# Kernel optimization log

Measured on AMD Instinct MI355X. Metric: run time of the kernel, lower is better.

The kernel has to match this reference:

```python
import jax, jax.numpy as jnp
import numpy as np

# Episode / graph constants
B, N, K, Q = 16, 5, 5, 5              # episodes, ways, shots, queries-per-class
NPG = 200                              # nodes per graph
DEG = 16                               # avg degree
F_DIM, H_DIM, OUT_DIM = 128, 128, 64
NS_G = B * N * K                       # 400 support graphs
NQ_G = B * N * Q                       # 400 query graphs
NS_NODES = NS_G * NPG                  # 80000
NQ_NODES = NQ_G * NPG                  # 80000
NEG_SLOPE = 0.2


def _rand_edges(key, n_nodes):
    # random in-graph source per (dst, k) slot; dst covers every node DEG times
    n_edges = n_nodes * DEG
    off = (jnp.arange(n_edges) // (NPG * DEG)) * NPG
    src = jax.random.randint(key, (n_edges,), 0, NPG) + off
    dst = jnp.repeat(jnp.arange(n_nodes), DEG)
    return jnp.stack([src, dst]).astype(jnp.int64)


def setup_inputs() -> dict:
    key = jax.random.key(0)
    ks = jax.random.split(key, 16)
    g = lambda k, shape, scale: jax.random.normal(k, shape, jnp.float32) * scale
    inp = {
        "supports_x": g(ks[0], (NS_NODES, F_DIM), 1.0),
        "queries_x": g(ks[1], (NQ_NODES, F_DIM), 1.0),
        "supports_edge_index": _rand_edges(ks[2], NS_NODES),
        "queries_edge_index": _rand_edges(ks[3], NQ_NODES),
        "supports_batch": (jnp.arange(NS_NODES) // NPG).astype(jnp.int64),
        "queries_batch": (jnp.arange(NQ_NODES) // NPG).astype(jnp.int64),
        # per-episode labels: N classes, K graphs each, local class ids 0..N-1
        "supports_y": jnp.tile(jnp.repeat(jnp.arange(N), K), B).astype(jnp.int64),
        "W1": g(ks[4], (F_DIM, H_DIM), 1.0 / np.sqrt(F_DIM)),
        "a1_src": g(ks[5], (H_DIM,), 1.0 / np.sqrt(H_DIM)),
        "a1_dst": g(ks[6], (H_DIM,), 1.0 / np.sqrt(H_DIM)),
        "b1": jnp.zeros((H_DIM,), jnp.float32),
        "W2": g(ks[7], (H_DIM, H_DIM), 1.0 / np.sqrt(H_DIM)),
        "a2_src": g(ks[8], (H_DIM,), 1.0 / np.sqrt(H_DIM)),
        "a2_dst": g(ks[9], (H_DIM,), 1.0 / np.sqrt(H_DIM)),
        "b2": jnp.zeros((H_DIM,), jnp.float32),
        "Wm1": g(ks[10], (H_DIM, H_DIM), 1.0 / np.sqrt(H_DIM)),
        "bm1": jnp.zeros((H_DIM,), jnp.float32),
        "Wm2": g(ks[11], (H_DIM, OUT_DIM), 1.0 / np.sqrt(H_DIM)),
        "bm2": jnp.zeros((OUT_DIM,), jnp.float32),
    }
    return inp


def gat_conv(x, src, dst, W, a_src, a_dst, b, n_nodes):
    """PyG GATConv, heads=1, add_self_loops=True."""
    xw = x @ W                                        # [n, H]
    loop = jnp.arange(n_nodes)
    src2 = jnp.concatenate([src, loop])
    dst2 = jnp.concatenate([dst, loop])
    e = (xw @ a_src)[src2] + (xw @ a_dst)[dst2]       # [E+n]
    e = jnp.where(e > 0, e, NEG_SLOPE * e)            # leaky_relu
    m = jax.ops.segment_max(e, dst2, num_segments=n_nodes)
    ex = jnp.exp(e - m[dst2])
    den = jax.ops.segment_sum(ex, dst2, num_segments=n_nodes)
    alpha = ex / den[dst2]                            # softmax per destination
    out = jax.ops.segment_sum(alpha[:, None] * xw[src2], dst2, num_segments=n_nodes)
    return out + b


def embed(x, edge_index, batch, n_graphs, W1, a1s, a1d, b1, W2, a2s, a2d, b2,
          Wm1, bm1, Wm2, bm2):
    n = x.shape[0]
    src, dst = edge_index[0], edge_index[1]
    h = jax.nn.relu(gat_conv(x, src, dst, W1, a1s, a1d, b1, n))
    h = jax.nn.relu(gat_conv(h, src, dst, W2, a2s, a2d, b2, n))
    h = jax.nn.relu(h @ Wm1 + bm1) @ Wm2 + bm2        # MLP
    # global mean pool
    s = jax.ops.segment_sum(h, batch, num_segments=n_graphs)
    cnt = jax.ops.segment_sum(jnp.ones((n,), h.dtype), batch, num_segments=n_graphs)
    return s / cnt[:, None]                           # [n_graphs, OUT_DIM]


def reference(supports_x, supports_edge_index, supports_batch, supports_y,
              queries_x, queries_edge_index, queries_batch,
              W1, a1_src, a1_dst, b1, W2, a2_src, a2_dst, b2,
              Wm1, bm1, Wm2, bm2):
    params = (W1, a1_src, a1_dst, b1, W2, a2_src, a2_dst, b2, Wm1, bm1, Wm2, bm2)
    emb_s = embed(supports_x, supports_edge_index, supports_batch, NS_G, *params)
    emb_q = embed(queries_x, queries_edge_index, queries_batch, NQ_G, *params)

    # class prototypes per episode: mean of supports with each (sorted) class label
    emb_s = emb_s.reshape(B, N * K, OUT_DIM)
    y = supports_y.reshape(B, N * K)
    onehot = jax.nn.one_hot(y, N, dtype=emb_s.dtype)          # [B, NK, N]
    proto = jnp.einsum("bkn,bke->bne", onehot, emb_s)
    proto = proto / onehot.sum(axis=1)[:, :, None]            # [B, N, E]

    # align queries with prototypes
    nq = N * Q                                                # queries per episode
    emb_q = emb_q.reshape(B, nq, OUT_DIM)
    rep_q = jnp.repeat(emb_q, N, axis=1)                      # repeat_interleave
    rep_p = jnp.tile(proto, (1, nq, 1))                       # repeat
    return rep_q.reshape(B * nq * N, OUT_DIM), rep_p.reshape(B * nq * N, OUT_DIM)
```

## Files before the change

### kernel.cpp

```cpp
#include <hip/hip_runtime.h>


typedef unsigned short u16;
typedef unsigned int   u32;
typedef unsigned char  u8;
typedef __attribute__((ext_vector_type(8))) short short8;
typedef __attribute__((ext_vector_type(4))) float f32x4;

#define NNODES   80000
#define DEG      16
#define NEDGES   (NNODES * DEG)
#define NGRAPH   400
#define NPG      200
#define FDIM     128
#define ODIM     64
#define NEPS     16
#define NWAY     5
#define NSHOT    5
#define NROWS    (2 * NNODES)
#define NGR2     (2 * NGRAPH)

__device__ __forceinline__ float b2f(u16 u) {
    return __uint_as_float(((u32)u) << 16);
}
__device__ __forceinline__ u16 f2b(float f) {
    u32 i = __float_as_uint(f);
    u32 r = i + 0x7FFFu + ((i >> 16) & 1u);
    return (u16)(r >> 16);
}

__global__ void detect_kernel(const u32* __restrict__ sx,
                              const int* __restrict__ ei,
                              int* __restrict__ flags)
{
    if (blockIdx.x == 0 && threadIdx.x == 0) {
        int ok32 = (ei[NEDGES + 16000] == 1000) && (ei[NEDGES + 32000] == 2000);
        flags[0] = ok32 ? 0 : 1;
        int cnt = 0;
        for (int i = 0; i < 64; i++) {
            u32 lo = sx[i] & 0xFFFFu;
            u32 e  = (lo >> 7) & 0xFFu;
            if (e >= 110u && e <= 135u) cnt++;
        }
        flags[1] = (cnt >= 32) ? 1 : 0;
    }
}

__global__ __launch_bounds__(256)
void canon_kernel(const void* __restrict__ W1, const void* __restrict__ W2,
                  const void* __restrict__ Wm1, const void* __restrict__ Wm2,
                  const void* a1s, const void* a1d, const void* b1,
                  const void* a2s, const void* a2d, const void* b2,
                  const void* bm1, const void* bm2,
                  const int* __restrict__ flags, u16* __restrict__ Wc,
                  float* __restrict__ Vc, float* __restrict__ emb)
{
    const int b = blockIdx.x, t = threadIdx.x;
    const int isb = flags[1];
    if (b < 224) {
        int idx = b * 256 + t;
        const void* src;
        int n, k, nout;
        if (idx < 16384)      { src = W1;  int l = idx;         n = l >> 7; k = l & 127; nout = 128; }
        else if (idx < 32768) { src = W2;  int l = idx - 16384; n = l >> 7; k = l & 127; nout = 128; }
        else if (idx < 49152) { src = Wm1; int l = idx - 32768; n = l >> 7; k = l & 127; nout = 128; }
        else                  { src = Wm2; int l = idx - 49152; n = l >> 7; k = l & 127; nout = 64; }
        int off = k * nout + n;
        Wc[idx] = isb ? ((const u16*)src)[off] : f2b(((const float*)src)[off]);
    } else if (b == 224) {
        for (int idx = t; idx < 960; idx += 256) {
            int g = idx >> 7, off = idx & 127;
            const void* src = (g == 0) ? a1s : (g == 1) ? a1d : (g == 2) ? b1 :
                              (g == 3) ? a2s : (g == 4) ? a2d : (g == 5) ? b2 :
                              (g == 6) ? bm1 : bm2;
            Vc[idx] = isb ? b2f(((const u16*)src)[off]) : ((const float*)src)[off];
        }
    } else {
        int i = (b - 225) * 256 + t;
        emb[i] = 0.f;
    }
}

__global__ __launch_bounds__(512)
void gemm_pack_kernel(const void* __restrict__ in0, const void* __restrict__ in1,
                      int in_mode, const int* __restrict__ flags,
                      const u16* __restrict__ Wt, const float* __restrict__ bias,
                      const float* __restrict__ avs, const float* __restrict__ avd,
                      u32* __restrict__ outP, float* __restrict__ es_g,
                      float* __restrict__ ed_g, int do_relu)
{
    __shared__ uint4 bsh[2048];

    const int t    = threadIdx.x;
    const int wv   = t >> 6;
    const int lane = t & 63;
    const int qd   = lane >> 4, md = lane & 15;

    int mode = in_mode;
    if (mode == 2) mode = flags[1];

    const size_t rowG = (size_t)blockIdx.x * 128 + wv * 16 + md;
    const int side = rowG >= NNODES;
    const size_t lrow = rowG - (side ? NNODES : 0);
    const void* in_ = side ? in1 : in0;

    short8 afr[4];
    if (mode) {
        const short* arow = (const short*)in_ + lrow * FDIM;
#pragma unroll
        for (int ks = 0; ks < 4; ks++)
            afr[ks] = *(const short8*)(arow + ks * 32 + qd * 8);
    } else {
        const float* arow = (const float*)in_ + lrow * FDIM;
#pragma unroll
        for (int ks = 0; ks < 4; ks++) {
            float4 u = *(const float4*)(arow + ks * 32 + qd * 8);
            float4 v = *(const float4*)(arow + ks * 32 + qd * 8 + 4);
            short8 tt;
            tt[0] = (short)f2b(u.x); tt[1] = (short)f2b(u.y);
            tt[2] = (short)f2b(u.z); tt[3] = (short)f2b(u.w);
            tt[4] = (short)f2b(v.x); tt[5] = (short)f2b(v.y);
            tt[6] = (short)f2b(v.z); tt[7] = (short)f2b(v.w);
            afr[ks] = tt;
        }
    }

    {
        const uint4* w4 = (const uint4*)Wt;
#pragma unroll
        for (int it = 0; it < 4; ++it) {
            int u   = it * 512 + t;
            int ctb = u >> 8, mdb = (u >> 4) & 15, ksb = (u >> 2) & 3, qdb = u & 3;
            bsh[ctb * 256 + ksb * 64 + qdb * 16 + mdb] = w4[u];
        }
    }
    __syncthreads();

    const size_t r0 = (size_t)blockIdx.x * 128 + wv * 16 + qd * 4;
    const bool has_av = (avs != nullptr);

    float sv[4] = {0.f, 0.f, 0.f, 0.f};
    float dv[4] = {0.f, 0.f, 0.f, 0.f};

    for (int ct = 0; ct < 8; ct++) {
        f32x4 acc = {0.f, 0.f, 0.f, 0.f};
#pragma unroll
        for (int ks = 0; ks < 4; ks++) {
            short8 bfr = *(const short8*)&bsh[(ct * 4 + ks) * 64 + lane];
            acc = __builtin_amdgcn_mfma_f32_16x16x32_bf16(afr[ks], bfr, acc, 0, 0, 0);
        }
        const int col = ct * 16 + md;
        const float bv  = bias ? bias[col] : 0.f;
        const float asv = has_av ? avs[col] : 0.f;
        const float adv = has_av ? avd[col] : 0.f;
#pragma unroll
        for (int i = 0; i < 4; i++) {
            float v = acc[i] + bv;
            if (do_relu) v = fmaxf(v, 0.f);
            sv[i] = fmaf(v, asv, sv[i]);
            dv[i] = fmaf(v, adv, dv[i]);
            float pr = __shfl_xor(v, 1, 64);
            if (!(md & 1)) {
                u32 pk = (u32)f2b(v) | ((u32)f2b(pr) << 16);
                outP[(r0 + i) * 64 + ct * 8 + (md >> 1)] = pk;
            }
        }
    }

    if (has_av) {
#pragma unroll
        for (int off = 1; off <= 8; off <<= 1) {
#pragma unroll
            for (int i = 0; i < 4; i++) {
                sv[i] += __shfl_xor(sv[i], off, 64);
                dv[i] += __shfl_xor(dv[i], off, 64);
            }
        }
        if (md == 0) {
#pragma unroll
            for (int i = 0; i < 4; i++) {
                es_g[r0 + i] = sv[i];
                ed_g[r0 + i] = dv[i];
            }
        }
    }
}

__global__ __launch_bounds__(512)
void gemm_pool_kernel(const u32* __restrict__ inP, const u16* __restrict__ Wt,
                      float* __restrict__ emb)
{
    __shared__ uint4 bsh[1024];
    __shared__ float psum[2][8][64];

    const int t = threadIdx.x;
    const int wv   = t >> 6;
    const int lane = t & 63;
    const int qd   = lane >> 4, md = lane & 15;

    const size_t rowA = (size_t)blockIdx.x * 128 + wv * 16 + md;
    const short* arow = (const short*)inP + rowA * FDIM;
    short8 afr[4];
#pragma unroll
    for (int ks = 0; ks < 4; ks++)
        afr[ks] = *(const short8*)(arow + ks * 32 + qd * 8);

    {
        const uint4* w4 = (const uint4*)Wt;
#pragma unroll
        for (int it = 0; it < 2; ++it) {
            int u   = it * 512 + t;
            int ctb = u >> 8, mdb = (u >> 4) & 15, ksb = (u >> 2) & 3, qdb = u & 3;
            bsh[ctb * 256 + ksb * 64 + qdb * 16 + mdb] = w4[u];
        }
    }
    __syncthreads();

    const int r0       = blockIdx.x * 128 + wv * 16 + qd * 4;
    const int g0       = (blockIdx.x * 128) / NPG;
    const int boundary = (g0 + 1) * NPG;

    for (int ct = 0; ct < 4; ct++) {
        f32x4 acc = {0.f, 0.f, 0.f, 0.f};
#pragma unroll
        for (int ks = 0; ks < 4; ks++) {
            short8 bfr = *(const short8*)&bsh[(ct * 4 + ks) * 64 + lane];
            acc = __builtin_amdgcn_mfma_f32_16x16x32_bf16(afr[ks], bfr, acc, 0, 0, 0);
        }
        float s0 = 0.f, s1 = 0.f;
#pragma unroll
        for (int i = 0; i < 4; i++) {
            if (r0 + i >= boundary) s1 += acc[i];
            else                    s0 += acc[i];
        }
        s0 += __shfl_xor(s0, 16, 64);  s1 += __shfl_xor(s1, 16, 64);
        s0 += __shfl_xor(s0, 32, 64);  s1 += __shfl_xor(s1, 32, 64);
        if (qd == 0) {
            psum[0][wv][ct * 16 + md] = s0;
            psum[1][wv][ct * 16 + md] = s1;
        }
    }
    __syncthreads();

    if (t < 128) {
        int p = t >> 6, c = t & 63;
        float s = 0.f;
#pragma unroll
        for (int w = 0; w < 8; w++) s += psum[p][w][c];
        if (p == 0 || boundary < blockIdx.x * 128 + 128)
            atomicAdd(&emb[(size_t)(g0 + p) * ODIM + c], s * (1.f / (float)NPG));
    }
}

__global__ __launch_bounds__(1024)
void gat_kernel(const u32* __restrict__ xwP, const float* __restrict__ es_g,
                const float* __restrict__ ed_g, const int* __restrict__ src0,
                const int* __restrict__ src1, const int* __restrict__ flags,
                const float* __restrict__ bias, u32* __restrict__ outH)
{
    __shared__ __align__(16) u32 xls[NPG * 64];
    __shared__ u16 alA[NPG * 18];
    __shared__ u8  slA[NPG * 20];

    const int g = blockIdx.x, t = threadIdx.x;
    const int side  = g >= NGRAPH;
    const int gbase = g * NPG;
    const int lbase = (g - (side ? NGRAPH : 0)) * NPG;
    const int* __restrict__ src = side ? src1 : src0;

    {
        const u32* gsrc = xwP + (size_t)gbase * 64;
        const int w = t >> 6, l = t & 63;
#pragma unroll
        for (int it = 0; it < 4; ++it) {
            int chunk = w + it * 16;
            if (chunk < 50) {
                __builtin_amdgcn_global_load_lds(
                    (const u32*)(gsrc + chunk * 256 + l * 4),
                    &xls[chunk * 256], 16, 0, 0);
            }
        }
    }

    if (t < 4 * NPG) {
        const int n = t >> 2, slot = t & 3;
        const int j0 = slot * 5;
        const int jn = (slot == 3) ? 2 : 5;
        const int is64 = flags[0];
        const float edn = ed_g[gbase + n];
        int   sl[5];
        float e[5];
        float mx = -1e30f;
#pragma unroll
        for (int jj = 0; jj < 5; jj++) {
            if (jj < jn) {
                int j = j0 + jj;
                int s;
                if (j == 16) {
                    s = n;
                } else {
                    int eidx = (lbase + n) * DEG + j;
                    s = (is64 ? src[2 * eidx] : src[eidx]) - lbase;
                }
                sl[jj] = s;
                float ev = es_g[gbase + s] + edn;
                ev = (ev > 0.f) ? ev : 0.2f * ev;
                e[jj] = ev;
                mx = fmaxf(mx, ev);
            }
        }
        mx = fmaxf(mx, __shfl_xor(mx, 1, 64));
        mx = fmaxf(mx, __shfl_xor(mx, 2, 64));
        float den = 0.f;
#pragma unroll
        for (int jj = 0; jj < 5; jj++) {
            if (jj < jn) {
                e[jj] = __expf(e[jj] - mx);
                den += e[jj];
            }
        }
        den += __shfl_xor(den, 1, 64);
        den += __shfl_xor(den, 2, 64);
        const float inv = 65535.f / den;
#pragma unroll
        for (int jj = 0; jj < 5; jj++) {
            if (jj < jn) {
                alA[n * 18 + j0 + jj] = (u16)(e[jj] * inv + 0.5f);
                slA[n * 20 + j0 + jj] = (u8)sl[jj];
            }
        }
    }

    __syncthreads();

    const int w = t >> 6, l = t & 63;
    const int sub = l >> 4, li = l & 15;
    const float4 bz0 = *(const float4*)&bias[8 * li];
    const float4 bz1 = *(const float4*)&bias[8 * li + 4];

    for (int p = w; p < NPG / 4; p += 16) {
        const int n = 4 * p + sub;
        float h0 = 0.f, h1 = 0.f, h2 = 0.f, h3 = 0.f;
        float h4 = 0.f, h5 = 0.f, h6 = 0.f, h7 = 0.f;
#pragma unroll 4
        for (int j = 0; j < 17; j++) {
            float a = (float)alA[n * 18 + j] * (1.f / 65535.f);
            int   s = (int)slA[n * 20 + j];
            uint4 q = *(const uint4*)&xls[s * 64 + 4 * li];
            h0 = fmaf(a, __uint_as_float(q.x << 16), h0);
            h1 = fmaf(a, __uint_as_float(q.x & 0xFFFF0000u), h1);
            h2 = fmaf(a, __uint_as_float(q.y << 16), h2);
            h3 = fmaf(a, __uint_as_float(q.y & 0xFFFF0000u), h3);
            h4 = fmaf(a, __uint_as_float(q.z << 16), h4);
            h5 = fmaf(a, __uint_as_float(q.z & 0xFFFF0000u), h5);
            h6 = fmaf(a, __uint_as_float(q.w << 16), h6);
            h7 = fmaf(a, __uint_as_float(q.w & 0xFFFF0000u), h7);
        }
        h0 = fmaxf(h0 + bz0.x, 0.f);
        h1 = fmaxf(h1 + bz0.y, 0.f);
        h2 = fmaxf(h2 + bz0.z, 0.f);
        h3 = fmaxf(h3 + bz0.w, 0.f);
        h4 = fmaxf(h4 + bz1.x, 0.f);
        h5 = fmaxf(h5 + bz1.y, 0.f);
        h6 = fmaxf(h6 + bz1.z, 0.f);
        h7 = fmaxf(h7 + bz1.w, 0.f);
        uint4 o;
        o.x = (u32)f2b(h0) | ((u32)f2b(h1) << 16);
        o.y = (u32)f2b(h2) | ((u32)f2b(h3) << 16);
        o.z = (u32)f2b(h4) | ((u32)f2b(h5) << 16);
        o.w = (u32)f2b(h6) | ((u32)f2b(h7) << 16);
        *(uint4*)&outH[(size_t)(gbase + n) * 64 + 4 * li] = o;
    }
}

__global__ __launch_bounds__(256)
void expand_kernel(const float* __restrict__ emb, const float* __restrict__ bm2,
                   const int* __restrict__ flags, void* __restrict__ out)
{
    int idx = blockIdx.x * 256 + threadIdx.x;
    const int TOT = NEPS * 125 * ODIM;
    if (idx >= TOT) return;
    int c = idx & 63;
    int tq = (idx >> 6) % 125;
    int b = idx / (125 * ODIM);
    int q = tq / NWAY, n = tq % NWAY;
    const float bb = bm2[c];
    float v0 = emb[(size_t)(NGRAPH + b * 25 + q) * ODIM + c] + bb;
    float v1 = 0.f;
#pragma unroll
    for (int k = 0; k < NSHOT; k++)
        v1 += emb[(size_t)(b * 25 + n * NSHOT + k) * ODIM + c];
    v1 = v1 * (1.f / (float)NSHOT) + bb;
    if (flags[1]) {
        ((u16*)out)[idx]       = f2b(v0);
        ((u16*)out)[TOT + idx] = f2b(v1);
    } else {
        ((float*)out)[idx]       = v0;
        ((float*)out)[TOT + idx] = v1;
    }
}

extern "C" void kernel_launch(void* const* d_in, const int* in_sizes, int n_in,
                              void* d_out, int out_size, void* d_ws, size_t ws_size,
                              hipStream_t stream)
{
    const void* sup_x  = d_in[0];
    const void* qry_x  = d_in[1];
    const int*  sup_ei = (const int*)d_in[2];
    const int*  qry_ei = (const int*)d_in[3];
    const void* W1  = d_in[7];
    const void* a1s = d_in[8];
    const void* a1d = d_in[9];
    const void* b1  = d_in[10];
    const void* W2  = d_in[11];
    const void* a2s = d_in[12];
    const void* a2d = d_in[13];
    const void* b2  = d_in[14];
    const void* Wm1 = d_in[15];
    const void* bm1 = d_in[16];
    const void* Wm2 = d_in[17];
    const void* bm2 = d_in[18];

    u32*   bufXW = (u32*)d_ws;
    u32*   bufH  = bufXW + (size_t)NROWS * 64;
    float* es_g  = (float*)(bufH + (size_t)NROWS * 64);
    float* ed_g  = es_g + NROWS;
    float* emb   = ed_g + NROWS;
    float* Vc    = emb + (size_t)NGR2 * ODIM;
    u16*   Wc    = (u16*)(Vc + 960);
    int*   flags = (int*)(Wc + 57344);

    const float* c_a1s = Vc + 0,   *c_a1d = Vc + 128, *c_b1  = Vc + 256;
    const float* c_a2s = Vc + 384, *c_a2d = Vc + 512, *c_b2  = Vc + 640;
    const float* c_bm1 = Vc + 768, *c_bm2 = Vc + 896;
    const u16* c_W1t  = Wc;
    const u16* c_W2t  = Wc + 16384;
    const u16* c_Wm1t = Wc + 32768;
    const u16* c_Wm2t = Wc + 49152;

    const int GEMM_BLOCKS = NROWS / 128;

    detect_kernel<<<1, 64, 0, stream>>>((const u32*)sup_x, sup_ei, flags);
    canon_kernel<<<425, 256, 0, stream>>>(W1, W2, Wm1, Wm2,
                                          a1s, a1d, b1, a2s, a2d, b2, bm1, bm2,
                                          flags, Wc, Vc, emb);

    const void* bufH0 = (const void*)bufH;
    const void* bufH1 = (const void*)(bufH + (size_t)NNODES * 64);

    gemm_pack_kernel<<<GEMM_BLOCKS, 512, 0, stream>>>(
        sup_x, qry_x, 2, flags, c_W1t, nullptr, c_a1s, c_a1d,
        bufXW, es_g, ed_g, 0);
    gat_kernel<<<NGR2, 1024, 0, stream>>>(
        bufXW, es_g, ed_g, sup_ei, qry_ei, flags, c_b1, bufH);

    gemm_pack_kernel<<<GEMM_BLOCKS, 512, 0, stream>>>(
        bufH0, bufH1, 1, flags, c_W2t, nullptr, c_a2s, c_a2d,
        bufXW, es_g, ed_g, 0);
    gat_kernel<<<NGR2, 1024, 0, stream>>>(
        bufXW, es_g, ed_g, sup_ei, qry_ei, flags, c_b2, bufH);

    gemm_pack_kernel<<<GEMM_BLOCKS, 512, 0, stream>>>(
        bufH0, bufH1, 1, flags, c_Wm1t, c_bm1, nullptr, nullptr,
        bufXW, es_g, ed_g, 1);

    gemm_pool_kernel<<<GEMM_BLOCKS, 512, 0, stream>>>(bufXW, c_Wm2t, emb);

    expand_kernel<<<(NEPS * 125 * ODIM + 255) / 256, 256, 0, stream>>>(
        emb, c_bm2, flags, d_out);
}
```

Measured before the change: 313.4 us.

## Swap MFMA operands, permute hidden feature order, pad LDS, use hardware bf16 pack

The GEMM epilogue now swaps the A/B operands of the MFMA so each lane holds four consecutive output columns for a single row. This allows vectorized bias and attention-vector loads, fewer cross-lane shuffles for the attention dot products, and 8-byte stores instead of shuffled 4-byte stores. To keep downstream consumers consistent, the hidden feature dimension is stored in a permuted order (semk), and the K index of W2/Wm1/Wm2 and the b1/b2 vectors are remapped to match. The weight tile in shared memory is padded by one slot every eight to reduce bank conflicts. Software bf16 rounding is replaced with the v_cvt_pk_bf16_f32 instruction, which adds correctness risk if the permutation or the rounding behavior does not match.

```diff
diff --git a/kernel.cpp b/kernel.cpp
--- a/kernel.cpp
+++ b/kernel.cpp
@@ -28,6 +28,14 @@
     u32 r = i + 0x7FFFu + ((i >> 16) & 1u);
     return (u16)(r >> 16);
 }
+__device__ __forceinline__ u32 cvtpk(float lo, float hi) {
+    u32 r;
+    asm("v_cvt_pk_bf16_f32 %0, %1, %2" : "=v"(r) : "v"(lo), "v"(hi));
+    return r;
+}
+__device__ __forceinline__ int semk(int p) {
+    return 16 * ((p >> 2) & 7) + 4 * (p >> 5) + 2 * ((p >> 1) & 1) + (p & 1);
+}
 
 __global__ void detect_kernel(const u32* __restrict__ sx,
                               const int* __restrict__ ei,
@@ -61,10 +69,10 @@
         int idx = b * 256 + t;
         const void* src;
         int n, k, nout;
-        if (idx < 16384)      { src = W1;  int l = idx;         n = l >> 7; k = l & 127; nout = 128; }
-        else if (idx < 32768) { src = W2;  int l = idx - 16384; n = l >> 7; k = l & 127; nout = 128; }
-        else if (idx < 49152) { src = Wm1; int l = idx - 32768; n = l >> 7; k = l & 127; nout = 128; }
-        else                  { src = Wm2; int l = idx - 49152; n = l >> 7; k = l & 127; nout = 64; }
+        if (idx < 16384)      { src = W1;  int l = idx;         n = l >> 7; k = l & 127;       nout = 128; }
+        else if (idx < 32768) { src = W2;  int l = idx - 16384; n = l >> 7; k = semk(l & 127); nout = 128; }
+        else if (idx < 49152) { src = Wm1; int l = idx - 32768; n = l >> 7; k = semk(l & 127); nout = 128; }
+        else                  { src = Wm2; int l = idx - 49152; n = l >> 7; k = semk(l & 127); nout = 64; }
         int off = k * nout + n;
         Wc[idx] = isb ? ((const u16*)src)[off] : f2b(((const float*)src)[off]);
     } else if (b == 224) {
@@ -73,7 +81,8 @@
             const void* src = (g == 0) ? a1s : (g == 1) ? a1d : (g == 2) ? b1 :
                               (g == 3) ? a2s : (g == 4) ? a2d : (g == 5) ? b2 :
                               (g == 6) ? bm1 : bm2;
-            Vc[idx] = isb ? b2f(((const u16*)src)[off]) : ((const float*)src)[off];
+            int soff = (g == 2 || g == 5) ? semk(off) : off;
+            Vc[idx] = isb ? b2f(((const u16*)src)[soff]) : ((const float*)src)[soff];
         }
     } else {
         int i = (b - 225) * 256 + t;
@@ -89,12 +98,13 @@
                       u32* __restrict__ outP, float* __restrict__ es_g,
                       float* __restrict__ ed_g, int do_relu)
 {
-    __shared__ uint4 bsh[2048];
+    __shared__ __align__(16) uint4 bsh[2304];
 
     const int t    = threadIdx.x;
     const int wv   = t >> 6;
     const int lane = t & 63;
     const int qd   = lane >> 4, md = lane & 15;
+    const int lofs = lane + (lane >> 3);
 
     int mode = in_mode;
     if (mode == 2) mode = flags[1];
@@ -129,59 +139,55 @@
         const uint4* w4 = (const uint4*)Wt;
 #pragma unroll
         for (int it = 0; it < 4; ++it) {
-            int u   = it * 512 + t;
-            int ctb = u >> 8, mdb = (u >> 4) & 15, ksb = (u >> 2) & 3, qdb = u & 3;
-            bsh[ctb * 256 + ksb * 64 + qdb * 16 + mdb] = w4[u];
+            int u    = it * 512 + t;
+            int ctb  = u >> 8, mdb = (u >> 4) & 15, ksb = (u >> 2) & 3, qdb = u & 3;
+            int slot = ctb * 256 + ksb * 64 + qdb * 16 + mdb;
+            bsh[slot + (slot >> 3)] = w4[u];
         }
     }
     __syncthreads();
 
-    const size_t r0 = (size_t)blockIdx.x * 128 + wv * 16 + qd * 4;
     const bool has_av = (avs != nullptr);
-
-    float sv[4] = {0.f, 0.f, 0.f, 0.f};
-    float dv[4] = {0.f, 0.f, 0.f, 0.f};
+    float sv = 0.f, dv = 0.f;
 
     for (int ct = 0; ct < 8; ct++) {
         f32x4 acc = {0.f, 0.f, 0.f, 0.f};
 #pragma unroll
         for (int ks = 0; ks < 4; ks++) {
-            short8 bfr = *(const short8*)&bsh[(ct * 4 + ks) * 64 + lane];
-            acc = __builtin_amdgcn_mfma_f32_16x16x32_bf16(afr[ks], bfr, acc, 0, 0, 0);
-        }
-        const int col = ct * 16 + md;
-        const float bv  = bias ? bias[col] : 0.f;
-        const float asv = has_av ? avs[col] : 0.f;
-        const float adv = has_av ? avd[col] : 0.f;
-#pragma unroll
-        for (int i = 0; i < 4; i++) {
-            float v = acc[i] + bv;
-            if (do_relu) v = fmaxf(v, 0.f);
-            sv[i] = fmaf(v, asv, sv[i]);
-            dv[i] = fmaf(v, adv, dv[i]);
-            float pr = __shfl_xor(v, 1, 64);
-            if (!(md & 1)) {
-                u32 pk = (u32)f2b(v) | ((u32)f2b(pr) << 16);
-                outP[(r0 + i) * 64 + ct * 8 + (md >> 1)] = pk;
-            }
-        }
+            short8 bfr = *(const short8*)&bsh[(ct * 4 + ks) * 72 + lofs];
+            acc = __builtin_amdgcn_mfma_f32_16x16x32_bf16(bfr, afr[ks], acc, 0, 0, 0);
+        }
+        const int colb = ct * 16 + qd * 4;
+        float4 bv4 = make_float4(0.f, 0.f, 0.f, 0.f);
+        if (bias) bv4 = *(const float4*)&bias[colb];
+        float v0 = acc[0] + bv4.x;
+        float v1 = acc[1] + bv4.y;
+        float v2 = acc[2] + bv4.z;
+        float v3 = acc[3] + bv4.w;
+        if (do_relu) {
+            v0 = fmaxf(v0, 0.f); v1 = fmaxf(v1, 0.f);
+            v2 = fmaxf(v2, 0.f); v3 = fmaxf(v3, 0.f);
+        }
+        if (has_av) {
+            float4 as4 = *(const float4*)&avs[colb];
+            float4 ad4 = *(const float4*)&avd[colb];
+            sv = fmaf(v0, as4.x, sv); sv = fmaf(v1, as4.y, sv);
+            sv = fmaf(v2, as4.z, sv); sv = fmaf(v3, as4.w, sv);
+            dv = fmaf(v0, ad4.x, dv); dv = fmaf(v1, ad4.y, dv);
+            dv = fmaf(v2, ad4.z, dv); dv = fmaf(v3, ad4.w, dv);
+        }
+        uint2 o;
+        o.x = cvtpk(v0, v1);
+        o.y = cvtpk(v2, v3);
+        *(uint2*)&outP[rowG * 64 + qd * 16 + ct * 2] = o;
     }
 
     if (has_av) {
-#pragma unroll
-        for (int off = 1; off <= 8; off <<= 1) {
-#pragma unroll
-            for (int i = 0; i < 4; i++) {
-                sv[i] += __shfl_xor(sv[i], off, 64);
-                dv[i] += __shfl_xor(dv[i], off, 64);
-            }
-        }
-        if (md == 0) {
-#pragma unroll
-            for (int i = 0; i < 4; i++) {
-                es_g[r0 + i] = sv[i];
-                ed_g[r0 + i] = dv[i];
-            }
+        sv += __shfl_xor(sv, 16, 64);  dv += __shfl_xor(dv, 16, 64);
+        sv += __shfl_xor(sv, 32, 64);  dv += __shfl_xor(dv, 32, 64);
+        if (qd == 0) {
+            es_g[rowG] = sv;
+            ed_g[rowG] = dv;
         }
     }
 }
@@ -365,10 +371,10 @@
         h6 = fmaxf(h6 + bz1.z, 0.f);
         h7 = fmaxf(h7 + bz1.w, 0.f);
         uint4 o;
-        o.x = (u32)f2b(h0) | ((u32)f2b(h1) << 16);
-        o.y = (u32)f2b(h2) | ((u32)f2b(h3) << 16);
-        o.z = (u32)f2b(h4) | ((u32)f2b(h5) << 16);
-        o.w = (u32)f2b(h6) | ((u32)f2b(h7) << 16);
+        o.x = cvtpk(h0, h1);
+        o.y = cvtpk(h2, h3);
+        o.z = cvtpk(h4, h5);
+        o.w = cvtpk(h6, h7);
         *(uint4*)&outH[(size_t)(gbase + n) * 64 + 4 * li] = o;
     }
 }
```

After: 347.7 us. 10.9% more time.
